# Kernel tuning notes

Measured on AMD Instinct MI355X. Metric: run time of the kernel, lower is better.

Reference implementation:

```python
import jax, jax.numpy as jnp
import numpy as np

# dims: B faces, H heads, D channels per code, K=16 blade components, N codes
B, H, D, K = 8192, 8, 16, 16
N, DF = 4096, 16  # num_codebook_codes, frozen_codebook_size
EPS = 1e-6


def setup_inputs() -> dict:
    key = jax.random.key(0)
    k1, k2, k3, k4 = jax.random.split(key, 4)
    x = jax.random.normal(k1, (B, H * D, K), dtype=jnp.float32)
    frozen_codebook = jax.random.normal(k2, (N, DF, K), dtype=jnp.float32) / np.sqrt(DF).astype(np.float32)
    W_i = jax.random.normal(k3, (D, DF), dtype=jnp.float32) / np.sqrt(DF).astype(np.float32)
    W_o = jax.random.normal(k4, (D, D), dtype=jnp.float32) / np.sqrt(D).astype(np.float32)
    return {"x": x, "frozen_codebook": frozen_codebook, "W_i": W_i, "W_o": W_o}


def _equi_linear(W, t):
    # channel-mixing linear applied independently per blade component (equivariant)
    return jnp.einsum('oi,nik->nok', W, t)


def _scaler_gated_gelu(t):
    # gate all blade components by GELU of the scalar (index-0) component
    return t * jax.nn.gelu(t[..., :1])


def _codebook(frozen_codebook, W_i, W_o):
    h = _scaler_gated_gelu(_equi_linear(W_i, frozen_codebook))
    return _equi_linear(W_o, h)  # (N, D, K)


def _forward(x, frozen_codebook, W_i, W_o):
    sg = jax.lax.stop_gradient
    # b (h d) k -> (b h) (d k)
    xf = x.reshape(B, H, D, K).reshape(B * H, D * K)
    cb = _codebook(frozen_codebook, W_i, W_o).reshape(N, D * K)

    # cdist(p=2) argmin; argmin of squared distances is identical
    d2 = ((xf * xf).sum(-1, keepdims=True)
          - 2.0 * xf @ cb.T
          + (cb * cb).sum(-1)[None, :])
    i = jnp.argmin(sg(d2), axis=-1)  # (B*H,)
    e = cb[i]  # gather, differentiable w.r.t. codebook params

    # Householder rotation STE
    xn = jnp.linalg.norm(xf, axis=-1, keepdims=True)
    en = jnp.linalg.norm(e, axis=-1, keepdims=True)
    xd = sg(xf / jnp.maximum(xn, EPS))
    ed = sg(e / jnp.maximum(en, EPS))
    sd = xd + ed
    sd = sd / jnp.maximum(jnp.linalg.norm(sd, axis=-1, keepdims=True), EPS)
    r = (xf
         - 2.0 * sd * (sd * xf).sum(-1, keepdims=True)
         + 2.0 * ed * (xd * xf).sum(-1, keepdims=True))
    s = r * sg(en / jnp.maximum(xn, EPS))

    restore = lambda t: t.reshape(B, H, D, K).reshape(B, H * D, K)
    return restore(e), restore(s)


def reference(x, frozen_codebook, W_i, W_o):
    return _forward(x, frozen_codebook, W_i, W_o)
```

## Files before the change

kernel.cpp:

```cpp
#include <hip/hip_runtime.h>
#include <hip/hip_bf16.h>
#include <stdint.h>

#define Bq    8192
#define Hh    8
#define Dd    16
#define Kk    16
#define Nn    4096
#define DFf   16
#define ROWS  (Bq*Hh)
#define COLS  (Dd*Kk)
#define EPSF  1e-6f

typedef unsigned long long u64;
typedef unsigned int u32;
typedef __attribute__((ext_vector_type(8)))  short bf16x8;
typedef __attribute__((ext_vector_type(16))) float f32x16;

#define GLOAD_LDS(g, l) __builtin_amdgcn_global_load_lds( \
    (const __attribute__((address_space(1))) u32*)(g), \
    (__attribute__((address_space(3))) u32*)(l), 16, 0, 0)

__device__ __forceinline__ float dot4(float4 a, float4 b) {
    return fmaf(a.x, b.x, fmaf(a.y, b.y, fmaf(a.z, b.z, a.w * b.w)));
}
__device__ __forceinline__ float wave_sum(float v) {
    #pragma unroll
    for (int m = 32; m > 0; m >>= 1) v += __shfl_xor(v, m, 64);
    return v;
}
__device__ __forceinline__ u32 f32_sortable(float f) {
    u32 u = __float_as_uint(f);
    return (u & 0x80000000u) ? ~u : (u | 0x80000000u);
}
__device__ __forceinline__ u32 pk2(float a, float b) {
    union { __hip_bfloat162 h; u32 u; } v;
    v.h = __float22bfloat162_rn(make_float2(a, b));
    return v.u;
}
__device__ __forceinline__ void exact_rerank(const float* __restrict__ X,
                                             const float* __restrict__ CB,
                                             const float* __restrict__ xx,
                                             const float* __restrict__ cbn,
                                             int row, int col,
                                             u64* __restrict__ best) {
    const float4* xp = (const float4*)(X + (size_t)row * COLS);
    const float4* cp = (const float4*)(CB + (size_t)col * COLS);
    float d = 0.f;
    #pragma unroll 8
    for (int q = 0; q < 64; ++q) {
        float4 a = xp[q], b = cp[q];
        d = fmaf(a.x, b.x, d); d = fmaf(a.y, b.y, d);
        d = fmaf(a.z, b.z, d); d = fmaf(a.w, b.w, d);
    }
    float d2e = fmaf(-2.f, d, xx[row]) + cbn[col];
    u64 pk = ((u64)f32_sortable(d2e) << 32) | (u32)col;
    atomicMin(&best[row], pk);
}

__global__ __launch_bounds__(256) void k_prep(const float* __restrict__ X,
                                              short* __restrict__ Xh,
                                              float* __restrict__ xx,
                                              u64* __restrict__ best,
                                              u32* __restrict__ cbn_max) {
    int r    = blockIdx.x * 4 + (threadIdx.x >> 6);
    int lane = threadIdx.x & 63;
    float4 v = *reinterpret_cast<const float4*>(X + (size_t)r * COLS + lane * 4);
    uint2 p; p.x = pk2(v.x, v.y); p.y = pk2(v.z, v.w);
    *reinterpret_cast<uint2*>(Xh + (size_t)r * COLS + lane * 4) = p;
    float s = wave_sum(v.x*v.x + v.y*v.y + v.z*v.z + v.w*v.w);
    if (lane == 0) { xx[r] = s; best[r] = ~0ull; }
    if (blockIdx.x == 0 && threadIdx.x == 0) *cbn_max = 0u;
}

__global__ __launch_bounds__(256) void k_codebook(const float* __restrict__ fc,
                                                  const float* __restrict__ Wi,
                                                  const float* __restrict__ Wo,
                                                  float* __restrict__ CB,
                                                  short* __restrict__ CBf,
                                                  float* __restrict__ cbn,
                                                  float* __restrict__ cbn_f,
                                                  u32* __restrict__ cbn_max) {
    int n = blockIdx.x, tid = threadIdx.x;
    int o = tid >> 4, k = tid & 15;
    __shared__ float fcs[256], wis[256], wos[256], hs[256], sq[256];
    __shared__ short cvs_sh[256];
    fcs[tid] = fc[(size_t)n * 256 + tid];
    wis[tid] = Wi[tid];
    wos[tid] = Wo[tid];
    __syncthreads();
    float hp = 0.f;
    #pragma unroll
    for (int i = 0; i < 16; ++i) hp = fmaf(wis[o*16 + i], fcs[i*16 + k], hp);
    hs[tid] = hp;
    __syncthreads();
    float h0 = hs[o * 16];
    float x3 = h0 * h0 * h0;
    float inner = 0.7978845608028654f * fmaf(0.044715f, x3, h0);
    float g = 0.5f * h0 * (1.f + tanhf(inner));
    float hg = hp * g;
    __syncthreads();
    hs[tid] = hg;
    __syncthreads();
    float cv = 0.f;
    #pragma unroll
    for (int i = 0; i < 16; ++i) cv = fmaf(wos[o*16 + i], hs[i*16 + k], cv);
    CB[(size_t)n * 256 + tid] = cv;
    { union { __hip_bfloat16 h; short s; } c; c.h = __float2bfloat16(cv);
      cvs_sh[tid] = c.s; }
    sq[tid] = cv * cv;
    __syncthreads();
    #pragma unroll
    for (int st = 128; st > 0; st >>= 1) {
        if (tid < st) sq[tid] += sq[tid + st];
        __syncthreads();
    }
    if (tid == 0) {
        cbn[n] = sq[0];
        atomicMax(cbn_max, __float_as_uint(sq[0]));
        int tile = n >> 5, c = n & 31;
        int h = (c >> 2) & 1, r = (c & 3) | ((c >> 3) << 2);
        cbn_f[tile * 32 + h * 16 + r] = sq[0];
    }
    if (tid < 32) {
        int kc = tid;
        int tile = n >> 5, c = n & 31;
        int kstep = kc >> 1, h = kc & 1;
        size_t off = (size_t)tile * 8192 + kstep * 512 + h * 256 + c * 8;
        *reinterpret_cast<uint4*>(CBf + off) =
            *reinterpret_cast<const uint4*>(&cvs_sh[kc * 8]);
    }
}

__global__ __launch_bounds__(256, 2) void k_screen_fused(
        const short* __restrict__ Xh,
        const short* __restrict__ CBf,
        const float* __restrict__ X,
        const float* __restrict__ CB,
        const float* __restrict__ cbn,
        const float* __restrict__ cbn_f,
        const float* __restrict__ xx,
        u64* __restrict__ best,
        const u32* __restrict__ cbn_max) {
    __shared__ __align__(16) short Bs[3][8192];
    __shared__ float cbn_fs[Nn];

    const int tid  = threadIdx.x;
    const int lane = tid & 63;
    const int w    = tid >> 6;
    const int cl   = lane & 31;
    const int kh   = lane >> 5;
    const int bmBase = blockIdx.x * 128;
    const int myrow  = bmBase + w * 32 + cl;

#define STAGE(t_, buf) do { \
        int _t = (t_); \
        _Pragma("unroll") \
        for (int _i = 0; _i < 4; ++_i) { \
            int _f = _i * 4 + w; \
            const short* _g = CBf + (size_t)_t * 8192 + _f * 512 + lane * 8; \
            GLOAD_LDS(_g, &Bs[(buf)][_f * 512]); \
        } \
    } while (0)

    #pragma unroll
    for (int j = 0; j < 4; ++j)
        *reinterpret_cast<float4*>(&cbn_fs[tid * 16 + j * 4]) =
            *reinterpret_cast<const float4*>(&cbn_f[tid * 16 + j * 4]);

    bf16x8 af[16];
    {
        const short* ap = Xh + ((size_t)myrow << 8) + kh * 8;
        #pragma unroll
        for (int ks = 0; ks < 16; ++ks)
            af[ks] = *reinterpret_cast<const bf16x8*>(ap + ks * 16);
    }

    float dlt, rmin = 1e30f;
    {
        float xr = xx[myrow];
        dlt = fmaf(0.003f, sqrtf(xr * __uint_as_float(*cbn_max)), 0.01f);
    }

    __syncthreads();

    STAGE(0, 0); STAGE(1, 1); STAGE(2, 2);

    float g0 = 1e30f, g1 = 1e30f, g2 = 1e30f, g3 = 1e30f, g4 = 1e30f, g5 = 1e30f;
    u32   s0 = 0,     s1 = 0,     s2 = 0,     s3 = 0,     s4 = 0,     s5 = 0;

    int p = 0;

    for (int t = 0; t < 128; ++t) {
        asm volatile("s_waitcnt vmcnt(8)" ::: "memory");
        __builtin_amdgcn_sched_barrier(0);
        __builtin_amdgcn_s_barrier();
        __builtin_amdgcn_sched_barrier(0);

        f32x16 acc;
        #pragma unroll
        for (int r = 0; r < 16; ++r) acc[r] = 0.f;

        const short* Bt = &Bs[p][0];
        #pragma unroll
        for (int ks = 0; ks < 16; ++ks) {
            bf16x8 cf = *reinterpret_cast<const bf16x8*>(&Bt[ks * 512 + lane * 8]);
            acc = __builtin_amdgcn_mfma_f32_32x32x16_bf16(cf, af[ks], acc, 0, 0, 0);
        }

        float cbnv[16];
        #pragma unroll
        for (int q = 0; q < 4; ++q)
            *reinterpret_cast<float4*>(&cbnv[q * 4]) =
                *reinterpret_cast<const float4*>(&cbn_fs[t * 32 + kh * 16 + q * 4]);
        float gv[16], m = 1e30f;
        #pragma unroll
        for (int r = 0; r < 16; ++r) {
            gv[r] = fmaf(-2.f, acc[r], cbnv[r]);
            m = fminf(m, gv[r]);
        }
        m = fminf(m, __shfl_xor(m, 32, 64));
        rmin = fminf(rmin, m);
        float thr = rmin + dlt;
        #pragma unroll
        for (int r = 0; r < 16; ++r) {
            if (gv[r] <= thr) {
                u32 code = (u32)(t * 32 + (r & 3) + 8 * (r >> 2) + 4 * kh);
                float mg = g0; int mi = 0;
                if (g1 > mg) { mg = g1; mi = 1; }
                if (g2 > mg) { mg = g2; mi = 2; }
                if (g3 > mg) { mg = g3; mi = 3; }
                if (g4 > mg) { mg = g4; mi = 4; }
                if (g5 > mg) { mg = g5; mi = 5; }
                if (mg > thr) {
                    if      (mi == 0) { g0 = gv[r]; s0 = code; }
                    else if (mi == 1) { g1 = gv[r]; s1 = code; }
                    else if (mi == 2) { g2 = gv[r]; s2 = code; }
                    else if (mi == 3) { g3 = gv[r]; s3 = code; }
                    else if (mi == 4) { g4 = gv[r]; s4 = code; }
                    else              { g5 = gv[r]; s5 = code; }
                } else {
                    exact_rerank(X, CB, xx, cbn, myrow, (int)code, best);
                }
            }
        }

        __builtin_amdgcn_sched_barrier(0);
        __builtin_amdgcn_s_barrier();
        __builtin_amdgcn_sched_barrier(0);
        STAGE((t + 3) & 127, p);
        p = (p == 2) ? 0 : p + 1;
    }

    float thrF = rmin + dlt;
    if (g0 <= thrF) exact_rerank(X, CB, xx, cbn, myrow, (int)s0, best);
    if (g1 <= thrF) exact_rerank(X, CB, xx, cbn, myrow, (int)s1, best);
    if (g2 <= thrF) exact_rerank(X, CB, xx, cbn, myrow, (int)s2, best);
    if (g3 <= thrF) exact_rerank(X, CB, xx, cbn, myrow, (int)s3, best);
    if (g4 <= thrF) exact_rerank(X, CB, xx, cbn, myrow, (int)s4, best);
    if (g5 <= thrF) exact_rerank(X, CB, xx, cbn, myrow, (int)s5, best);
#undef STAGE
}

__global__ __launch_bounds__(256) void k_epilogue(const float* __restrict__ X,
                                                  const float* __restrict__ CB,
                                                  const u64* __restrict__ best,
                                                  float* __restrict__ Eout,
                                                  float* __restrict__ Sout) {
    int r    = blockIdx.x * 4 + (threadIdx.x >> 6);
    int lane = threadIdx.x & 63;
    int idx  = (int)(best[r] & 0xffffffffull);

    float4 xv = *reinterpret_cast<const float4*>(X  + (size_t)r   * COLS + lane * 4);
    float4 ev = *reinterpret_cast<const float4*>(CB + (size_t)idx * COLS + lane * 4);

    float xn2 = wave_sum(dot4(xv, xv));
    float en2 = wave_sum(dot4(ev, ev));
    float xn = sqrtf(xn2), en = sqrtf(en2);
    float invx = 1.f / fmaxf(xn, EPSF);
    float inve = 1.f / fmaxf(en, EPSF);

    float4 xd, ed, sd0;
    xd.x = xv.x*invx; xd.y = xv.y*invx; xd.z = xv.z*invx; xd.w = xv.w*invx;
    ed.x = ev.x*inve; ed.y = ev.y*inve; ed.z = ev.z*inve; ed.w = ev.w*inve;
    sd0.x = xd.x+ed.x; sd0.y = xd.y+ed.y; sd0.z = xd.z+ed.z; sd0.w = xd.w+ed.w;

    float sdn2 = wave_sum(dot4(sd0, sd0));
    float p1   = wave_sum(dot4(sd0, xv));
    float p2   = wave_sum(dot4(xd,  xv));
    float invs = 1.f / fmaxf(sqrtf(sdn2), EPSF);

    float csd = -2.f * invs * invs * p1;
    float ced =  2.f * p2;
    float4 rr;
    rr.x = fmaf(csd, sd0.x, fmaf(ced, ed.x, xv.x));
    rr.y = fmaf(csd, sd0.y, fmaf(ced, ed.y, xv.y));
    rr.z = fmaf(csd, sd0.z, fmaf(ced, ed.z, xv.z));
    rr.w = fmaf(csd, sd0.w, fmaf(ced, ed.w, xv.w));
    float sc = en * invx;
    float4 sv; sv.x = rr.x*sc; sv.y = rr.y*sc; sv.z = rr.z*sc; sv.w = rr.w*sc;

    *reinterpret_cast<float4*>(Eout + (size_t)r * COLS + lane * 4) = ev;
    *reinterpret_cast<float4*>(Sout + (size_t)r * COLS + lane * 4) = sv;
}

extern "C" void kernel_launch(void* const* d_in, const int* in_sizes, int n_in,
                              void* d_out, int out_size, void* d_ws, size_t ws_size,
                              hipStream_t stream) {
    const float* x  = (const float*)d_in[0];
    const float* fc = (const float*)d_in[1];
    const float* Wi = (const float*)d_in[2];
    const float* Wo = (const float*)d_in[3];

    char* ws = (char*)d_ws;
    u64*   best    = (u64*)ws;                            ws += (size_t)ROWS * 8;
    float* CBws    = (float*)ws;                          ws += (size_t)Nn * COLS * 4;
    float* cbn     = (float*)ws;                          ws += (size_t)Nn * 4;
    float* cbn_f   = (float*)ws;                          ws += (size_t)Nn * 4;
    float* xx      = (float*)ws;                          ws += (size_t)ROWS * 4;
    u32*   cbn_max = (u32*)ws;

    short* Xh  = (short*)d_out;
    short* CBf = (short*)((char*)d_out + (64u << 20));

    float* Eout = (float*)d_out;
    float* Sout = Eout + (size_t)ROWS * COLS;

    k_prep<<<ROWS / 4, 256, 0, stream>>>(x, Xh, xx, best, cbn_max);
    k_codebook<<<Nn, 256, 0, stream>>>(fc, Wi, Wo, CBws, CBf, cbn, cbn_f, cbn_max);
    k_screen_fused<<<ROWS / 128, 256, 0, stream>>>(Xh, CBf, x, CBws, cbn, cbn_f, xx, best, cbn_max);
    k_epilogue<<<ROWS / 4, 256, 0, stream>>>(x, CBws, best, Eout, Sout);
}
```

Before: 337.1 us.

## Process two codebook tiles per iteration with interleaved MFMA chains and double buffering

```diff
diff --git a/kernel.cpp b/kernel.cpp
--- a/kernel.cpp
+++ b/kernel.cpp
@@ -142,7 +142,7 @@
         const float* __restrict__ xx,
         u64* __restrict__ best,
         const u32* __restrict__ cbn_max) {
-    __shared__ __align__(16) short Bs[3][8192];
+    __shared__ __align__(16) short Bs[2][16384];
     __shared__ float cbn_fs[Nn];
 
     const int tid  = threadIdx.x;
@@ -153,13 +153,15 @@
     const int bmBase = blockIdx.x * 128;
     const int myrow  = bmBase + w * 32 + cl;
 
-#define STAGE(t_, buf) do { \
-        int _t = (t_); \
+#define STAGE2(P_, buf) do { \
+        int _P = (P_); \
         _Pragma("unroll") \
-        for (int _i = 0; _i < 4; ++_i) { \
-            int _f = _i * 4 + w; \
-            const short* _g = CBf + (size_t)_t * 8192 + _f * 512 + lane * 8; \
-            GLOAD_LDS(_g, &Bs[(buf)][_f * 512]); \
+        for (int _i = 0; _i < 8; ++_i) { \
+            int _half = _i >> 2; \
+            int _f = (_i & 3) * 4 + w; \
+            const short* _g = CBf + (size_t)(_P * 2 + _half) * 8192 \
+                            + _f * 512 + lane * 8; \
+            GLOAD_LDS(_g, &Bs[(buf)][_half * 8192 + _f * 512]); \
         } \
     } while (0)
 
@@ -184,72 +186,77 @@
 
     __syncthreads();
 
-    STAGE(0, 0); STAGE(1, 1); STAGE(2, 2);
+    STAGE2(0, 0); STAGE2(1, 1);
 
     float g0 = 1e30f, g1 = 1e30f, g2 = 1e30f, g3 = 1e30f, g4 = 1e30f, g5 = 1e30f;
     u32   s0 = 0,     s1 = 0,     s2 = 0,     s3 = 0,     s4 = 0,     s5 = 0;
 
-    int p = 0;
-
-    for (int t = 0; t < 128; ++t) {
+#define EPI(accv, tile_) do { \
+        int _t = (tile_); \
+        float cbnv[16]; \
+        _Pragma("unroll") \
+        for (int _q = 0; _q < 4; ++_q) \
+            *reinterpret_cast<float4*>(&cbnv[_q * 4]) = \
+                *reinterpret_cast<const float4*>(&cbn_fs[_t * 32 + kh * 16 + _q * 4]); \
+        float gv[16], _m = 1e30f; \
+        _Pragma("unroll") \
+        for (int _r = 0; _r < 16; ++_r) { \
+            gv[_r] = fmaf(-2.f, (accv)[_r], cbnv[_r]); \
+            _m = fminf(_m, gv[_r]); \
+        } \
+        _m = fminf(_m, __shfl_xor(_m, 32, 64)); \
+        rmin = fminf(rmin, _m); \
+        float _thr = rmin + dlt; \
+        _Pragma("unroll") \
+        for (int _r = 0; _r < 16; ++_r) { \
+            if (gv[_r] <= _thr) { \
+                u32 _code = (u32)(_t * 32 + (_r & 3) + 8 * (_r >> 2) + 4 * kh); \
+                float _mg = g0; int _mi = 0; \
+                if (g1 > _mg) { _mg = g1; _mi = 1; } \
+                if (g2 > _mg) { _mg = g2; _mi = 2; } \
+                if (g3 > _mg) { _mg = g3; _mi = 3; } \
+                if (g4 > _mg) { _mg = g4; _mi = 4; } \
+                if (g5 > _mg) { _mg = g5; _mi = 5; } \
+                if (_mg > _thr) { \
+                    if      (_mi == 0) { g0 = gv[_r]; s0 = _code; } \
+                    else if (_mi == 1) { g1 = gv[_r]; s1 = _code; } \
+                    else if (_mi == 2) { g2 = gv[_r]; s2 = _code; } \
+                    else if (_mi == 3) { g3 = gv[_r]; s3 = _code; } \
+                    else if (_mi == 4) { g4 = gv[_r]; s4 = _code; } \
+                    else               { g5 = gv[_r]; s5 = _code; } \
+                } else { \
+                    exact_rerank(X, CB, xx, cbn, myrow, (int)_code, best); \
+                } \
+            } \
+        } \
+    } while (0)
+
+    for (int s = 0; s < 64; ++s) {
         asm volatile("s_waitcnt vmcnt(8)" ::: "memory");
         __builtin_amdgcn_sched_barrier(0);
         __builtin_amdgcn_s_barrier();
         __builtin_amdgcn_sched_barrier(0);
 
-        f32x16 acc;
+        f32x16 aA, aB;
         #pragma unroll
-        for (int r = 0; r < 16; ++r) acc[r] = 0.f;
-
-        const short* Bt = &Bs[p][0];
+        for (int r = 0; r < 16; ++r) { aA[r] = 0.f; aB[r] = 0.f; }
+
+        const short* Bt = &Bs[s & 1][0];
         #pragma unroll
         for (int ks = 0; ks < 16; ++ks) {
-            bf16x8 cf = *reinterpret_cast<const bf16x8*>(&Bt[ks * 512 + lane * 8]);
-            acc = __builtin_amdgcn_mfma_f32_32x32x16_bf16(cf, af[ks], acc, 0, 0, 0);
+            bf16x8 cfA = *reinterpret_cast<const bf16x8*>(&Bt[ks * 512 + lane * 8]);
+            bf16x8 cfB = *reinterpret_cast<const bf16x8*>(&Bt[8192 + ks * 512 + lane * 8]);
+            aA = __builtin_amdgcn_mfma_f32_32x32x16_bf16(cfA, af[ks], aA, 0, 0, 0);
+            aB = __builtin_amdgcn_mfma_f32_32x32x16_bf16(cfB, af[ks], aB, 0, 0, 0);
         }
 
-        float cbnv[16];
-        #pragma unroll
-        for (int q = 0; q < 4; ++q)
-            *reinterpret_cast<float4*>(&cbnv[q * 4]) =
-                *reinterpret_cast<const float4*>(&cbn_fs[t * 32 + kh * 16 + q * 4]);
-        float gv[16], m = 1e30f;
-        #pragma unroll
-        for (int r = 0; r < 16; ++r) {
-            gv[r] = fmaf(-2.f, acc[r], cbnv[r]);
-            m = fminf(m, gv[r]);
-        }
-        m = fminf(m, __shfl_xor(m, 32, 64));
-        rmin = fminf(rmin, m);
-        float thr = rmin + dlt;
-        #pragma unroll
-        for (int r = 0; r < 16; ++r) {
-            if (gv[r] <= thr) {
-                u32 code = (u32)(t * 32 + (r & 3) + 8 * (r >> 2) + 4 * kh);
-                float mg = g0; int mi = 0;
-                if (g1 > mg) { mg = g1; mi = 1; }
-                if (g2 > mg) { mg = g2; mi = 2; }
-                if (g3 > mg) { mg = g3; mi = 3; }
-                if (g4 > mg) { mg = g4; mi = 4; }
-                if (g5 > mg) { mg = g5; mi = 5; }
-                if (mg > thr) {
-                    if      (mi == 0) { g0 = gv[r]; s0 = code; }
-                    else if (mi == 1) { g1 = gv[r]; s1 = code; }
-                    else if (mi == 2) { g2 = gv[r]; s2 = code; }
-                    else if (mi == 3) { g3 = gv[r]; s3 = code; }
-                    else if (mi == 4) { g4 = gv[r]; s4 = code; }
-                    else              { g5 = gv[r]; s5 = code; }
-                } else {
-                    exact_rerank(X, CB, xx, cbn, myrow, (int)code, best);
-                }
-            }
-        }
+        EPI(aA, s * 2);
+        EPI(aB, s * 2 + 1);
 
         __builtin_amdgcn_sched_barrier(0);
         __builtin_amdgcn_s_barrier();
         __builtin_amdgcn_sched_barrier(0);
-        STAGE((t + 3) & 127, p);
-        p = (p == 2) ? 0 : p + 1;
+        STAGE2((s + 2) & 63, s & 1);
     }
 
     float thrF = rmin + dlt;
@@ -259,7 +266,8 @@
     if (g3 <= thrF) exact_rerank(X, CB, xx, cbn, myrow, (int)s3, best);
     if (g4 <= thrF) exact_rerank(X, CB, xx, cbn, myrow, (int)s4, best);
     if (g5 <= thrF) exact_rerank(X, CB, xx, cbn, myrow, (int)s5, best);
-#undef STAGE
+#undef EPI
+#undef STAGE2
 }
 
 __global__ __launch_bounds__(256) void k_epilogue(const float* __restrict__ X,
```

Measured after the change: 324.4 us. -3.8%, faster.

## Split codebook scan across two blocks per row tile, double-buffer LDS

Applied to the files above, without the earlier changes.

```diff
diff --git a/kernel.cpp b/kernel.cpp
--- a/kernel.cpp
+++ b/kernel.cpp
@@ -61,8 +61,7 @@
 __global__ __launch_bounds__(256) void k_prep(const float* __restrict__ X,
                                               short* __restrict__ Xh,
                                               float* __restrict__ xx,
-                                              u64* __restrict__ best,
-                                              u32* __restrict__ cbn_max) {
+                                              u64* __restrict__ best) {
     int r    = blockIdx.x * 4 + (threadIdx.x >> 6);
     int lane = threadIdx.x & 63;
     float4 v = *reinterpret_cast<const float4*>(X + (size_t)r * COLS + lane * 4);
@@ -70,7 +69,6 @@
     *reinterpret_cast<uint2*>(Xh + (size_t)r * COLS + lane * 4) = p;
     float s = wave_sum(v.x*v.x + v.y*v.y + v.z*v.z + v.w*v.w);
     if (lane == 0) { xx[r] = s; best[r] = ~0ull; }
-    if (blockIdx.x == 0 && threadIdx.x == 0) *cbn_max = 0u;
 }
 
 __global__ __launch_bounds__(256) void k_codebook(const float* __restrict__ fc,
@@ -79,8 +77,7 @@
                                                   float* __restrict__ CB,
                                                   short* __restrict__ CBf,
                                                   float* __restrict__ cbn,
-                                                  float* __restrict__ cbn_f,
-                                                  u32* __restrict__ cbn_max) {
+                                                  float* __restrict__ cbn_f) {
     int n = blockIdx.x, tid = threadIdx.x;
     int o = tid >> 4, k = tid & 15;
     __shared__ float fcs[256], wis[256], wos[256], hs[256], sq[256];
@@ -117,7 +114,6 @@
     }
     if (tid == 0) {
         cbn[n] = sq[0];
-        atomicMax(cbn_max, __float_as_uint(sq[0]));
         int tile = n >> 5, c = n & 31;
         int h = (c >> 2) & 1, r = (c & 3) | ((c >> 3) << 2);
         cbn_f[tile * 32 + h * 16 + r] = sq[0];
@@ -132,7 +128,23 @@
     }
 }
 
-__global__ __launch_bounds__(256, 2) void k_screen_fused(
+__global__ __launch_bounds__(256) void k_reduce_cbn(const float* __restrict__ cbn,
+                                                    u32* __restrict__ cbn_max) {
+    __shared__ float sn[256];
+    int tid = threadIdx.x;
+    float cm = 0.f;
+    for (int i = tid; i < Nn; i += 256) cm = fmaxf(cm, cbn[i]);
+    sn[tid] = cm;
+    __syncthreads();
+    #pragma unroll
+    for (int st = 128; st > 0; st >>= 1) {
+        if (tid < st) sn[tid] = fmaxf(sn[tid], sn[tid + st]);
+        __syncthreads();
+    }
+    if (tid == 0) *cbn_max = __float_as_uint(sn[0]);
+}
+
+__global__ __launch_bounds__(256, 3) void k_screen_fused(
         const short* __restrict__ Xh,
         const short* __restrict__ CBf,
         const float* __restrict__ X,
@@ -142,19 +154,20 @@
         const float* __restrict__ xx,
         u64* __restrict__ best,
         const u32* __restrict__ cbn_max) {
-    __shared__ __align__(16) short Bs[3][8192];
-    __shared__ float cbn_fs[Nn];
+    __shared__ __align__(16) short Bs[2][8192];
 
     const int tid  = threadIdx.x;
     const int lane = tid & 63;
     const int w    = tid >> 6;
     const int cl   = lane & 31;
     const int kh   = lane >> 5;
-    const int bmBase = blockIdx.x * 128;
+    const int half = blockIdx.x & 1;
+    const int tgBase = half * 64;
+    const int bmBase = (blockIdx.x >> 1) * 128;
     const int myrow  = bmBase + w * 32 + cl;
 
-#define STAGE(t_, buf) do { \
-        int _t = (t_); \
+#define STAGE(tg_, buf) do { \
+        int _t = (tg_); \
         _Pragma("unroll") \
         for (int _i = 0; _i < 4; ++_i) { \
             int _f = _i * 4 + w; \
@@ -163,11 +176,6 @@
         } \
     } while (0)
 
-    #pragma unroll
-    for (int j = 0; j < 4; ++j)
-        *reinterpret_cast<float4*>(&cbn_fs[tid * 16 + j * 4]) =
-            *reinterpret_cast<const float4*>(&cbn_f[tid * 16 + j * 4]);
-
     bf16x8 af[16];
     {
         const short* ap = Xh + ((size_t)myrow << 8) + kh * 8;
@@ -182,37 +190,37 @@
         dlt = fmaf(0.003f, sqrtf(xr * __uint_as_float(*cbn_max)), 0.01f);
     }
 
-    __syncthreads();
-
-    STAGE(0, 0); STAGE(1, 1); STAGE(2, 2);
+    STAGE(tgBase, 0);
 
     float g0 = 1e30f, g1 = 1e30f, g2 = 1e30f, g3 = 1e30f, g4 = 1e30f, g5 = 1e30f;
     u32   s0 = 0,     s1 = 0,     s2 = 0,     s3 = 0,     s4 = 0,     s5 = 0;
 
-    int p = 0;
-
-    for (int t = 0; t < 128; ++t) {
-        asm volatile("s_waitcnt vmcnt(8)" ::: "memory");
+    for (int t = 0; t < 64; ++t) {
+        asm volatile("s_waitcnt vmcnt(0)" ::: "memory");
         __builtin_amdgcn_sched_barrier(0);
         __builtin_amdgcn_s_barrier();
         __builtin_amdgcn_sched_barrier(0);
 
+        STAGE(tgBase + ((t + 1) & 63), (t + 1) & 1);
+
+        float cbnv[16];
+        #pragma unroll
+        for (int q = 0; q < 4; ++q)
+            *reinterpret_cast<float4*>(&cbnv[q * 4]) =
+                *reinterpret_cast<const float4*>(
+                    &cbn_f[(tgBase + t) * 32 + kh * 16 + q * 4]);
+
         f32x16 acc;
         #pragma unroll
         for (int r = 0; r < 16; ++r) acc[r] = 0.f;
 
-        const short* Bt = &Bs[p][0];
+        const short* Bt = &Bs[t & 1][0];
         #pragma unroll
         for (int ks = 0; ks < 16; ++ks) {
             bf16x8 cf = *reinterpret_cast<const bf16x8*>(&Bt[ks * 512 + lane * 8]);
             acc = __builtin_amdgcn_mfma_f32_32x32x16_bf16(cf, af[ks], acc, 0, 0, 0);
         }
 
-        float cbnv[16];
-        #pragma unroll
-        for (int q = 0; q < 4; ++q)
-            *reinterpret_cast<float4*>(&cbnv[q * 4]) =
-                *reinterpret_cast<const float4*>(&cbn_fs[t * 32 + kh * 16 + q * 4]);
         float gv[16], m = 1e30f;
         #pragma unroll
         for (int r = 0; r < 16; ++r) {
@@ -225,7 +233,7 @@
         #pragma unroll
         for (int r = 0; r < 16; ++r) {
             if (gv[r] <= thr) {
-                u32 code = (u32)(t * 32 + (r & 3) + 8 * (r >> 2) + 4 * kh);
+                u32 code = (u32)((tgBase + t) * 32 + (r & 3) + 8 * (r >> 2) + 4 * kh);
                 float mg = g0; int mi = 0;
                 if (g1 > mg) { mg = g1; mi = 1; }
                 if (g2 > mg) { mg = g2; mi = 2; }
@@ -244,12 +252,6 @@
                 }
             }
         }
-
-        __builtin_amdgcn_sched_barrier(0);
-        __builtin_amdgcn_s_barrier();
-        __builtin_amdgcn_sched_barrier(0);
-        STAGE((t + 3) & 127, p);
-        p = (p == 2) ? 0 : p + 1;
     }
 
     float thrF = rmin + dlt;
@@ -326,8 +328,10 @@
     float* Eout = (float*)d_out;
     float* Sout = Eout + (size_t)ROWS * COLS;
 
-    k_prep<<<ROWS / 4, 256, 0, stream>>>(x, Xh, xx, best, cbn_max);
-    k_codebook<<<Nn, 256, 0, stream>>>(fc, Wi, Wo, CBws, CBf, cbn, cbn_f, cbn_max);
-    k_screen_fused<<<ROWS / 128, 256, 0, stream>>>(Xh, CBf, x, CBws, cbn, cbn_f, xx, best, cbn_max);
+    k_prep<<<ROWS / 4, 256, 0, stream>>>(x, Xh, xx, best);
+    k_codebook<<<Nn, 256, 0, stream>>>(fc, Wi, Wo, CBws, CBf, cbn, cbn_f);
+    k_reduce_cbn<<<1, 256, 0, stream>>>(cbn, cbn_max);
+    k_screen_fused<<<(ROWS / 128) * 2, 256, 0, stream>>>(Xh, CBf, x, CBws, cbn,
+                                                         cbn_f, xx, best, cbn_max);
     k_epilogue<<<ROWS / 4, 256, 0, stream>>>(x, CBws, best, Eout, Sout);
 }
```

Result: slower. 422.8 us (+25.4%).
